# Performance work log

Hardware: AMD Instinct MI355X
Metric: run time of the kernel (lower is better)

## Reference

```python
import jax, jax.numpy as jnp
import numpy as np

RADIUS2 = 0.03 ** 2
SIM_THRESH = 0.7
EPS = 1e-8


def setup_inputs() -> dict:
    key = jax.random.key(0)
    k1, k2, k3, k4, k5, k6, k7 = jax.random.split(key, 7)
    B, N, D = 2, 6144, 32
    # points in a 0.3-side cube so radius 0.03 gives realistic neighbor counts
    points = jax.random.uniform(k1, (B, N, 3), dtype=jnp.float32) * 0.3
    embeddings = jax.random.normal(k2, (B, N, D), dtype=jnp.float32)
    leaf_mask = jax.random.randint(k3, (B, N), 0, 2, dtype=jnp.int32)
    # consistency_net: Linear(2D, D) -> ReLU -> Linear(D, D)
    W1 = jax.random.normal(k4, (2 * D, D), dtype=jnp.float32) * (1.0 / np.sqrt(2 * D))
    b1 = jax.random.normal(k5, (D,), dtype=jnp.float32) * 0.01
    W2 = jax.random.normal(k6, (D, D), dtype=jnp.float32) * (1.0 / np.sqrt(D))
    b2 = jax.random.normal(k7, (D,), dtype=jnp.float32) * 0.01
    return {"points": points, "embeddings": embeddings, "leaf_mask": leaf_mask,
            "W1": W1, "b1": b1, "W2": W2, "b2": b2}


def reference(points, embeddings, leaf_mask, W1, b1, W2, b2):
    # points: [B,N,3], embeddings: [B,N,D], leaf_mask: [B,N] int (0/1)
    dt = embeddings.dtype
    leaf = leaf_mask > 0  # [B,N] bool

    # pairwise squared distances via the Gram trick (avoids [B,N,N,3])
    pn = jnp.sum(points * points, axis=-1)                      # [B,N]
    gram = jnp.einsum('bic,bjc->bij', points, points)           # [B,N,N]
    d2 = jnp.maximum(pn[:, :, None] + pn[:, None, :] - 2.0 * gram, 0.0)

    # neighbor mask: within radius AND neighbor is leaf (matches dist<0.03 & leaf_mask)
    nb = (d2 < RADIUS2) & leaf[:, None, :]                      # [B,N,N]

    # cosine similarity with torch's eps clamp on norms
    enorm = jnp.maximum(jnp.linalg.norm(embeddings, axis=-1), EPS)  # [B,N]
    inner = jnp.einsum('bid,bjd->bij', embeddings, embeddings)      # [B,N,N]
    sims = inner / (enorm[:, :, None] * enorm[:, None, :])

    sim_mask = nb & (sims > SIM_THRESH)                          # [B,N,N]
    cnt_nb = jnp.sum(nb, axis=-1)                                # [B,N]
    cnt_sim = jnp.sum(sim_mask, axis=-1)                         # [B,N]

    # mean of similar-neighbor embeddings
    sum_sim = jnp.einsum('bij,bjd->bid', sim_mask.astype(dt), embeddings)
    mean_sim = sum_sim / jnp.maximum(cnt_sim, 1).astype(dt)[..., None]

    # consistency MLP on [center_embedding, mean_similar]
    combined = jnp.concatenate([embeddings, mean_sim], axis=-1)  # [B,N,2D]
    h = jax.nn.relu(jnp.einsum('bnk,kd->bnd', combined, W1) + b1)
    out = jnp.einsum('bnk,kd->bnd', h, W2) + b2                  # [B,N,D]

    # refine only leaf points with >1 neighbor and >0 similar neighbors
    cond = leaf & (cnt_nb > 1) & (cnt_sim > 0)                   # [B,N]
    refined = jnp.where(cond[..., None], out, embeddings)

    # per-batch early exit: sum(leaf_mask) < 10 -> unchanged
    batch_ok = jnp.sum(leaf_mask, axis=-1) >= 10                 # [B]
    return jnp.where(batch_ok[:, None, None], refined, embeddings)
```

## Files before the change

kernel.cpp:

```cpp
#include <hip/hip_runtime.h>

#define NPTS    6144
#define DIM     32
#define NB      2
#define NCELL   1000
#define R2      0.0009f
#define NWAVES  4
#define BLOCK   (NWAVES * 64)
#define LEAFBIT 8192
#define PPT     6
#define NBCAP   128

__device__ __forceinline__ int cellof(float x) {
    int c = (int)(x * (10.0f / 0.3f));
    return min(max(c, 0), 9);
}

#define WS_LEAF   0
#define WS_CSTART 4
#define WS_SORTED 2008

__global__ __launch_bounds__(1024)
void build_cells(const float* __restrict__ points, const int* __restrict__ leaf,
                 int* __restrict__ ws)
{
    __shared__ int s_hist[1024];
    __shared__ int s_cursor[1024];
    __shared__ int s_wsum[16];
    __shared__ int s_leaf;

    const int t = threadIdx.x;
    const int b = blockIdx.x;
    const int w = t >> 6, lane = t & 63;

    s_hist[t] = 0;
    if (t == 0) s_leaf = 0;

    float px[PPT], py[PPT], pz[PPT];
    int   pc[PPT], pw[PPT];

    __syncthreads();

    int lc = 0;
    #pragma unroll
    for (int r = 0; r < PPT; ++r) {
        const int i  = r * 1024 + t;
        const int gi = b * NPTS + i;
        px[r] = points[gi * 3 + 0];
        py[r] = points[gi * 3 + 1];
        pz[r] = points[gi * 3 + 2];
        const int lf = leaf[gi] > 0 ? 1 : 0;
        lc += lf;
        pc[r] = (cellof(pz[r]) * 10 + cellof(py[r])) * 10 + cellof(px[r]);
        pw[r] = i + (lf ? LEAFBIT : 0);
        atomicAdd(&s_hist[pc[r]], 1);
    }
    #pragma unroll
    for (int off = 32; off > 0; off >>= 1) lc += __shfl_down(lc, off);
    if (lane == 0) atomicAdd(&s_leaf, lc);
    __syncthreads();

    const int v = s_hist[t];
    int x = v;
    #pragma unroll
    for (int off = 1; off < 64; off <<= 1) {
        const int y = __shfl_up(x, off);
        if (lane >= off) x += y;
    }
    if (lane == 63) s_wsum[w] = x;
    __syncthreads();
    if (t < 16) {
        int wv = s_wsum[t];
        #pragma unroll
        for (int off = 1; off < 16; off <<= 1) {
            const int y = __shfl_up(wv, off);
            if (t >= off) wv += y;
        }
        s_wsum[t] = wv;
    }
    __syncthreads();
    const int incl = x + (w > 0 ? s_wsum[w - 1] : 0);
    s_cursor[t] = incl - v;

    if (t < NCELL) ws[WS_CSTART + b * (NCELL + 1) + t + 1] = incl;
    if (t == 0) {
        ws[WS_CSTART + b * (NCELL + 1)] = 0;
        ws[WS_LEAF + b] = s_leaf;
    }
    __syncthreads();

    float4* sorted = (float4*)(ws + WS_SORTED) + (size_t)b * NPTS;
    #pragma unroll
    for (int r = 0; r < PPT; ++r) {
        const int pos = atomicAdd(&s_cursor[pc[r]], 1);
        sorted[pos] = make_float4(px[r], py[r], pz[r], (float)pw[r]);
    }
}

__global__ __launch_bounds__(BLOCK)
void refine(const float* __restrict__ emb,
            const float* __restrict__ W1, const float* __restrict__ b1,
            const float* __restrict__ W2, const float* __restrict__ b2,
            const int* __restrict__ ws, float* __restrict__ out)
{
    __shared__ __align__(16) float s_ei[NWAVES][DIM];
    __shared__ float s_ssum[NWAVES][DIM];
    __shared__ float s_h[NWAVES][DIM];
    __shared__ int   s_nb[NWAVES][NBCAP];

    const int tid  = threadIdx.x;
    const int wid  = tid >> 6;
    const int lane = tid & 63;
    const int s    = blockIdx.x * NWAVES + wid;
    const int b    = s / NPTS;
    const int slot = s - b * NPTS;

    const float4* srt  = (const float4*)(ws + WS_SORTED) + (size_t)b * NPTS;
    const int*    cst  = ws + WS_CSTART + b * (NCELL + 1);
    const float*  embB = emb + (size_t)b * NPTS * DIM;

    const float4 P  = srt[slot];
    const int    iw = (int)P.w;
    const int    io = iw & (LEAFBIT - 1);
    const bool   li = (iw & LEAFBIT) != 0;

    if (lane < DIM) {
        s_ei[wid][lane]   = embB[(size_t)io * DIM + lane];
        s_ssum[wid][lane] = 0.0f;
    }

    float ni2 = 0.0f;
    #pragma unroll
    for (int d = 0; d < DIM; ++d) { const float v = s_ei[wid][d]; ni2 += v * v; }
    const float rni = 1.0f / fmaxf(sqrtf(ni2), 1e-8f);

    const int cx = cellof(P.x), cy = cellof(P.y), cz = cellof(P.z);

    int begv = 0, lenv = 0;
    if (lane < 9) {
        const int z = cz + lane / 3 - 1;
        const int y = cy + lane % 3 - 1;
        if ((unsigned)z <= 9u && (unsigned)y <= 9u) {
            const int rowb = (z * 10 + y) * 10;
            const int c0   = rowb + max(cx - 1, 0);
            const int c1   = rowb + min(cx + 1, 9);
            begv = cst[c0];
            lenv = cst[c1 + 1] - begv;
        }
    }
    const int rb0 = __shfl(begv, 0), rb1 = __shfl(begv, 1), rb2 = __shfl(begv, 2);
    const int rb3 = __shfl(begv, 3), rb4 = __shfl(begv, 4), rb5 = __shfl(begv, 5);
    const int rb6 = __shfl(begv, 6), rb7 = __shfl(begv, 7), rb8 = __shfl(begv, 8);
    const int ln0 = __shfl(lenv, 0), ln1 = __shfl(lenv, 1), ln2 = __shfl(lenv, 2);
    const int ln3 = __shfl(lenv, 3), ln4 = __shfl(lenv, 4), ln5 = __shfl(lenv, 5);
    const int ln6 = __shfl(lenv, 6), ln7 = __shfl(lenv, 7), ln8 = __shfl(lenv, 8);
    const int pf1 = ln0,       pf2 = pf1 + ln1, pf3 = pf2 + ln2;
    const int pf4 = pf3 + ln3, pf5 = pf4 + ln4, pf6 = pf5 + ln5;
    const int pf7 = pf6 + ln6, pf8 = pf7 + ln7, pf9 = pf8 + ln8;

    int nbcnt = 0;
    for (int base = 0; base < pf9; base += 64) {
        const int g = base + lane;
        int j = 0;
        if (g < pf9) j = rb8 + g - pf8;
        if (g < pf8) j = rb7 + g - pf7;
        if (g < pf7) j = rb6 + g - pf6;
        if (g < pf6) j = rb5 + g - pf5;
        if (g < pf5) j = rb4 + g - pf4;
        if (g < pf4) j = rb3 + g - pf3;
        if (g < pf3) j = rb2 + g - pf2;
        if (g < pf2) j = rb1 + g - pf1;
        if (g < pf1) j = rb0 + g;
        const float4 Q  = srt[j];
        const float dx = Q.x - P.x, dy = Q.y - P.y, dz = Q.z - P.z;
        const float d2 = dx * dx + dy * dy + dz * dz;
        const int   jw = (int)Q.w;
        const bool  nb = (g < pf9) && (d2 < R2) && ((jw & LEAFBIT) != 0);
        const unsigned long long m = __ballot(nb);
        if (nb) {
            const int pos = nbcnt + __popcll(m & ((1ull << lane) - 1ull));
            if (pos < NBCAP) s_nb[wid][pos] = jw & (LEAFBIT - 1);
        }
        nbcnt += __popcll(m);
    }
    const int cnt_nb = nbcnt;

    int csim = 0;
    const int nh = min(cnt_nb, NBCAP);
    for (int h0 = 0; h0 < nh; h0 += 64) {
        const int h = h0 + lane;
        bool surv = false;
        float ejr[DIM];
        if (h < nh) {
            const int jo = s_nb[wid][h];
            const float4* ej4 = (const float4*)(embB + (size_t)jo * DIM);
            #pragma unroll
            for (int k = 0; k < DIM / 4; ++k) {
                const float4 v = ej4[k];
                ejr[4 * k + 0] = v.x; ejr[4 * k + 1] = v.y;
                ejr[4 * k + 2] = v.z; ejr[4 * k + 3] = v.w;
            }
            float dot = 0.0f, nj2 = 0.0f;
            #pragma unroll
            for (int d = 0; d < DIM; ++d) {
                dot += s_ei[wid][d] * ejr[d];
                nj2 += ejr[d] * ejr[d];
            }
            const float rnj = 1.0f / fmaxf(sqrtf(nj2), 1e-8f);
            surv = (dot * rni * rnj) > 0.7f;
        }
        csim += __popcll(__ballot(surv));
        if (surv) {
            #pragma unroll
            for (int d = 0; d < DIM; ++d)
                atomicAdd(&s_ssum[wid][d], ejr[d]);
        }
    }

    const bool ok   = ws[WS_LEAF + b] >= 10;
    const bool cond = ok && li && (cnt_nb > 1) && (csim > 0);

    float* outp = out + ((size_t)b * NPTS + io) * DIM;
    if (lane < DIM) {
        if (!cond) {
            outp[lane] = s_ei[wid][lane];
        } else {
            s_ssum[wid][lane] = s_ssum[wid][lane] / (float)csim;
            float acc = b1[lane];
            for (int k = 0; k < DIM; ++k)
                acc = fmaf(s_ei[wid][k],   W1[k * DIM + lane], acc);
            for (int k = 0; k < DIM; ++k)
                acc = fmaf(s_ssum[wid][k], W1[(DIM + k) * DIM + lane], acc);
            s_h[wid][lane] = fmaxf(acc, 0.0f);
            float acc2 = b2[lane];
            for (int k = 0; k < DIM; ++k)
                acc2 = fmaf(s_h[wid][k], W2[k * DIM + lane], acc2);
            outp[lane] = acc2;
        }
    }
}

extern "C" void kernel_launch(void* const* d_in, const int* in_sizes, int n_in,
                              void* d_out, int out_size, void* d_ws, size_t ws_size,
                              hipStream_t stream) {
    const float* points = (const float*)d_in[0];
    const float* emb    = (const float*)d_in[1];
    const int*   leaf   = (const int*)d_in[2];
    const float* W1     = (const float*)d_in[3];
    const float* b1     = (const float*)d_in[4];
    const float* W2     = (const float*)d_in[5];
    const float* b2     = (const float*)d_in[6];
    float*       outp   = (float*)d_out;
    int*         ws     = (int*)d_ws;

    build_cells<<<NB, 1024, 0, stream>>>(points, leaf, ws);

    const int grid = (NB * NPTS) / NWAVES;
    refine<<<grid, BLOCK, 0, stream>>>(emb, W1, b1, W2, b2, ws, outp);
}
```

Baseline: 91.20 us.

## Replace shared atomics with survivor list and stage MLP weights in LDS

Similar-neighbor accumulation no longer uses per-element shared atomicAdds. Each wave compacts the indices of surviving neighbors into a shared list, then lanes 0-31 sum those rows, one dimension each. The MLP weights and biases are copied into LDS once per block, and the MLP loops are unrolled with two accumulators. The cost is a block-wide sync, about 12KB more LDS per block and re-reading survivor embeddings from global memory. The survivor list is capped at NBCAP, the same bound already used for the neighbor list.

```diff
diff --git a/kernel.cpp b/kernel.cpp
--- a/kernel.cpp
+++ b/kernel.cpp
@@ -104,9 +104,13 @@
             const int* __restrict__ ws, float* __restrict__ out)
 {
     __shared__ __align__(16) float s_ei[NWAVES][DIM];
-    __shared__ float s_ssum[NWAVES][DIM];
+    __shared__ float s_mean[NWAVES][DIM];
     __shared__ float s_h[NWAVES][DIM];
     __shared__ int   s_nb[NWAVES][NBCAP];
+    __shared__ int   s_sv[NWAVES][NBCAP];
+    __shared__ __align__(16) float s_W1[2 * DIM * DIM];
+    __shared__ __align__(16) float s_W2[DIM * DIM];
+    __shared__ float s_b1[DIM], s_b2[DIM];
 
     const int tid  = threadIdx.x;
     const int wid  = tid >> 6;
@@ -119,15 +123,25 @@
     const int*    cst  = ws + WS_CSTART + b * (NCELL + 1);
     const float*  embB = emb + (size_t)b * NPTS * DIM;
 
+    {
+        const float4* w1v = (const float4*)W1;
+        float4*       sw1 = (float4*)s_W1;
+        for (int idx = tid; idx < (2 * DIM * DIM) / 4; idx += BLOCK) sw1[idx] = w1v[idx];
+        const float4* w2v = (const float4*)W2;
+        float4*       sw2 = (float4*)s_W2;
+        for (int idx = tid; idx < (DIM * DIM) / 4; idx += BLOCK) sw2[idx] = w2v[idx];
+        if (tid < DIM) { s_b1[tid] = b1[tid]; s_b2[tid] = b2[tid]; }
+    }
+
     const float4 P  = srt[slot];
     const int    iw = (int)P.w;
     const int    io = iw & (LEAFBIT - 1);
     const bool   li = (iw & LEAFBIT) != 0;
-
-    if (lane < DIM) {
-        s_ei[wid][lane]   = embB[(size_t)io * DIM + lane];
-        s_ssum[wid][lane] = 0.0f;
-    }
+    const bool   ok = ws[WS_LEAF + b] >= 10;
+
+    if (lane < DIM) s_ei[wid][lane] = embB[(size_t)io * DIM + lane];
+
+    __syncthreads();
 
     float ni2 = 0.0f;
     #pragma unroll
@@ -190,34 +204,36 @@
     for (int h0 = 0; h0 < nh; h0 += 64) {
         const int h = h0 + lane;
         bool surv = false;
-        float ejr[DIM];
+        int  jo   = 0;
         if (h < nh) {
-            const int jo = s_nb[wid][h];
+            jo = s_nb[wid][h];
             const float4* ej4 = (const float4*)(embB + (size_t)jo * DIM);
+            float dot = 0.0f, nj2 = 0.0f;
             #pragma unroll
             for (int k = 0; k < DIM / 4; ++k) {
                 const float4 v = ej4[k];
-                ejr[4 * k + 0] = v.x; ejr[4 * k + 1] = v.y;
-                ejr[4 * k + 2] = v.z; ejr[4 * k + 3] = v.w;
-            }
-            float dot = 0.0f, nj2 = 0.0f;
-            #pragma unroll
-            for (int d = 0; d < DIM; ++d) {
-                dot += s_ei[wid][d] * ejr[d];
-                nj2 += ejr[d] * ejr[d];
+                const float4 a = *(const float4*)&s_ei[wid][4 * k];
+                dot += a.x * v.x + a.y * v.y + a.z * v.z + a.w * v.w;
+                nj2 += v.x * v.x + v.y * v.y + v.z * v.z + v.w * v.w;
             }
             const float rnj = 1.0f / fmaxf(sqrtf(nj2), 1e-8f);
             surv = (dot * rni * rnj) > 0.7f;
         }
-        csim += __popcll(__ballot(surv));
+        const unsigned long long m = __ballot(surv);
         if (surv) {
-            #pragma unroll
-            for (int d = 0; d < DIM; ++d)
-                atomicAdd(&s_ssum[wid][d], ejr[d]);
-        }
-    }
-
-    const bool ok   = ws[WS_LEAF + b] >= 10;
+            const int pos = csim + __popcll(m & ((1ull << lane) - 1ull));
+            s_sv[wid][pos] = jo;
+        }
+        csim += __popcll(m);
+    }
+
+    if (lane < DIM) {
+        float msum = 0.0f;
+        for (int v = 0; v < csim; ++v)
+            msum += embB[(size_t)s_sv[wid][v] * DIM + lane];
+        s_mean[wid][lane] = (csim > 0) ? msum / (float)csim : 0.0f;
+    }
+
     const bool cond = ok && li && (cnt_nb > 1) && (csim > 0);
 
     float* outp = out + ((size_t)b * NPTS + io) * DIM;
@@ -225,17 +241,25 @@
         if (!cond) {
             outp[lane] = s_ei[wid][lane];
         } else {
-            s_ssum[wid][lane] = s_ssum[wid][lane] / (float)csim;
-            float acc = b1[lane];
-            for (int k = 0; k < DIM; ++k)
-                acc = fmaf(s_ei[wid][k],   W1[k * DIM + lane], acc);
-            for (int k = 0; k < DIM; ++k)
-                acc = fmaf(s_ssum[wid][k], W1[(DIM + k) * DIM + lane], acc);
-            s_h[wid][lane] = fmaxf(acc, 0.0f);
-            float acc2 = b2[lane];
-            for (int k = 0; k < DIM; ++k)
-                acc2 = fmaf(s_h[wid][k], W2[k * DIM + lane], acc2);
-            outp[lane] = acc2;
+            float a0 = s_b1[lane], a1 = 0.0f;
+            #pragma unroll
+            for (int k = 0; k < DIM; k += 2) {
+                a0 = fmaf(s_ei[wid][k],     s_W1[k * DIM + lane],       a0);
+                a1 = fmaf(s_ei[wid][k + 1], s_W1[(k + 1) * DIM + lane], a1);
+            }
+            #pragma unroll
+            for (int k = 0; k < DIM; k += 2) {
+                a0 = fmaf(s_mean[wid][k],     s_W1[(DIM + k) * DIM + lane],     a0);
+                a1 = fmaf(s_mean[wid][k + 1], s_W1[(DIM + k + 1) * DIM + lane], a1);
+            }
+            s_h[wid][lane] = fmaxf(a0 + a1, 0.0f);
+            float c0 = s_b2[lane], c1 = 0.0f;
+            #pragma unroll
+            for (int k = 0; k < DIM; k += 2) {
+                c0 = fmaf(s_h[wid][k],     s_W2[k * DIM + lane],       c0);
+                c1 = fmaf(s_h[wid][k + 1], s_W2[(k + 1) * DIM + lane], c1);
+            }
+            outp[lane] = c0 + c1;
         }
     }
 }
```

After: 92.64 us. Within noise of the previous version (+1.6%).
